# Kernel optimization log

Hardware: AMD Instinct MI355X
Metric: run time of the kernel (lower is better)

## Reference

```python
import jax, jax.numpy as jnp
import numpy as np

B, S, E, H = 4, 2048, 1024, 16
D = E // H  # head dim = 64


def setup_inputs() -> dict:
    key = jax.random.key(0)
    ks = jax.random.split(key, 9)
    s_in = 1.0 / np.sqrt(E)
    return {
        "x": jax.random.normal(ks[0], (B, S, E), dtype=jnp.float32),
        # stacked per-head projection weights, acting as x @ W + b
        "Wq": jax.random.normal(ks[1], (H, E, D), dtype=jnp.float32) * s_in,
        "bq": jax.random.normal(ks[2], (H, D), dtype=jnp.float32) * 0.01,
        "Wk": jax.random.normal(ks[3], (H, E, D), dtype=jnp.float32) * s_in,
        "bk": jax.random.normal(ks[4], (H, D), dtype=jnp.float32) * 0.01,
        "Wv": jax.random.normal(ks[5], (H, E, D), dtype=jnp.float32) * s_in,
        "bv": jax.random.normal(ks[6], (H, D), dtype=jnp.float32) * 0.01,
        "Wo": jax.random.normal(ks[7], (E, E), dtype=jnp.float32) * s_in,
        "bo": jax.random.normal(ks[8], (E,), dtype=jnp.float32) * 0.01,
    }


def reference(x, Wq, bq, Wk, bk, Wv, bv, Wo, bo):
    # Batched per-head projections (equivalent to the per-head nn.Linear loop)
    q = jnp.einsum("bse,hed->bhsd", x, Wq) + bq[None, :, None, :]
    k = jnp.einsum("bse,hed->bhsd", x, Wk) + bk[None, :, None, :]
    v = jnp.einsum("bse,hed->bhsd", x, Wv) + bv[None, :, None, :]
    scale = 1.0 / jnp.sqrt(jnp.asarray(D, dtype=x.dtype))
    scores = jnp.einsum("bhsd,bhtd->bhst", q, k) * scale  # [B,H,S,S]
    attn = jax.nn.softmax(scores, axis=-1)
    ctx = jnp.einsum("bhst,bhtd->bhsd", attn, v)  # [B,H,S,D]
    # torch.cat over heads along last dim -> [B,S,H*D]=[B,S,E]
    ctx = jnp.transpose(ctx, (0, 2, 1, 3)).reshape(x.shape[0], x.shape[1], E)
    return ctx @ Wo + bo
```

## Files before the change

### kernel.cpp

```cpp
#include <hip/hip_runtime.h>
#include <math.h>

#define B_ 4
#define S_ 2048
#define E_ 1024
#define H_ 16
#define D_ 64
#define BH_ (B_ * H_)

#define SCALE_LOG2E 0.18033688011112042f

typedef short short8 __attribute__((ext_vector_type(8)));
typedef float f32x4 __attribute__((ext_vector_type(4)));

static __device__ __forceinline__ unsigned short f2bf(float f) {
    unsigned int u = __float_as_uint(f);
    unsigned int r = (u + 0x7fffu + ((u >> 16) & 1u)) >> 16;
    return (unsigned short)r;
}

static __device__ __forceinline__ unsigned int pack_bf16_trunc(float hi, float lo) {
    return __builtin_amdgcn_perm(__float_as_uint(hi), __float_as_uint(lo), 0x07060302u);
}

static __device__ __forceinline__ void gl_lds16(const unsigned short* g, unsigned short* l) {
    __builtin_amdgcn_global_load_lds(
        (const __attribute__((address_space(1))) unsigned int*)g,
        (__attribute__((address_space(3))) unsigned int*)l, 16, 0, 0);
}


__global__ __launch_bounds__(256) void xcvt_kernel(
    const float* __restrict__ x, unsigned short* __restrict__ Xb)
{
    size_t i = ((size_t)blockIdx.x * 256 + threadIdx.x) * 8;
    float4 a = *(const float4*)&x[i];
    float4 b = *(const float4*)&x[i + 4];
    ushort4 u0, u1;
    u0.x = f2bf(a.x); u0.y = f2bf(a.y); u0.z = f2bf(a.z); u0.w = f2bf(a.w);
    u1.x = f2bf(b.x); u1.y = f2bf(b.y); u1.z = f2bf(b.z); u1.w = f2bf(b.w);
    *(ushort4*)&Xb[i]     = u0;
    *(ushort4*)&Xb[i + 4] = u1;
}

__global__ __launch_bounds__(256) void wtrans_kernel(
    const float* __restrict__ src, unsigned short* __restrict__ dst,
    int R, int C, int srcZ, int dstZ, float scale)
{
    __shared__ float t[32][33];
    const int tx = threadIdx.x & 31, ty = threadIdx.x >> 5;
    const int r0 = blockIdx.x * 32, c0 = blockIdx.y * 32, z = blockIdx.z;
    const float* s = src + (size_t)z * srcZ;
    unsigned short* d = dst + (size_t)z * dstZ;
#pragma unroll
    for (int i = 0; i < 4; ++i)
        t[ty + i * 8][tx] = s[(size_t)(r0 + ty + i * 8) * C + c0 + tx];
    __syncthreads();
#pragma unroll
    for (int i = 0; i < 4; ++i)
        d[(size_t)(c0 + ty + i * 8) * R + r0 + tx] = f2bf(t[tx][ty + i * 8] * scale);
}

__global__ __launch_bounds__(256) void qkv_gemm_kernel(
    const unsigned short* __restrict__ Xb, const unsigned short* __restrict__ Wt,
    const float* __restrict__ bq, const float* __restrict__ bk,
    const float* __restrict__ bv,
    unsigned short* __restrict__ Qh, unsigned short* __restrict__ Kh,
    unsigned short* __restrict__ Vth)
{
    __shared__ unsigned short As[2][128 * 64];
    __shared__ unsigned short Bs[2][128 * 64];
    const int tid = threadIdx.x;
    const int lane = tid & 63, wid = tid >> 6;
    const int quad = lane >> 4, lc = lane & 15;
    const int wm = wid >> 1, wn = wid & 1;
    const int m0 = blockIdx.y * 128, n0 = blockIdx.x * 128;
    const int l8 = lane >> 3;
    const int sch = ((lane & 7) ^ l8) * 8;

    f32x4 acc[4][4];
#pragma unroll
    for (int mt = 0; mt < 4; ++mt)
#pragma unroll
        for (int nt = 0; nt < 4; ++nt)
            acc[mt][nt] = (f32x4){0.f, 0.f, 0.f, 0.f};

#pragma unroll
    for (int i = 0; i < 4; ++i) {
        int rw = wid * 32 + i * 8;
        gl_lds16(&Xb[(size_t)(m0 + rw + l8) * E_ + sch], &As[0][rw * 64]);
        gl_lds16(&Wt[(size_t)(n0 + rw + l8) * E_ + sch], &Bs[0][rw * 64]);
    }
    __syncthreads();

    for (int k0 = 0; k0 < E_; k0 += 64) {
        const int cur = (k0 >> 6) & 1;
        if (k0 + 64 < E_) {
#pragma unroll
            for (int i = 0; i < 4; ++i) {
                int rw = wid * 32 + i * 8;
                gl_lds16(&Xb[(size_t)(m0 + rw + l8) * E_ + k0 + 64 + sch], &As[cur ^ 1][rw * 64]);
                gl_lds16(&Wt[(size_t)(n0 + rw + l8) * E_ + k0 + 64 + sch], &Bs[cur ^ 1][rw * 64]);
            }
        }
#pragma unroll
        for (int kc = 0; kc < 2; ++kc) {
            short8 a[4], bfr[4];
#pragma unroll
            for (int mt = 0; mt < 4; ++mt)
                a[mt] = *(const short8*)&As[cur][(wm * 64 + mt * 16 + lc) * 64 +
                                                (((kc * 4 + quad) ^ (lc & 7)) << 3)];
#pragma unroll
            for (int nt = 0; nt < 4; ++nt)
                bfr[nt] = *(const short8*)&Bs[cur][(wn * 64 + nt * 16 + lc) * 64 +
                                                  (((kc * 4 + quad) ^ (lc & 7)) << 3)];
#pragma unroll
            for (int mt = 0; mt < 4; ++mt)
#pragma unroll
                for (int nt = 0; nt < 4; ++nt)
                    acc[mt][nt] = __builtin_amdgcn_mfma_f32_16x16x32_bf16(
                        a[mt], bfr[nt], acc[mt][nt], 0, 0, 0);
        }
        __syncthreads();
    }

    const int nb = n0 + wn * 64;
    const int mtx = nb >> 10;
    const int h = (nb >> 6) & 15;
    const int sg0 = m0 + wm * 64;
    const int bb_ = sg0 >> 11;
    if (mtx < 2) {
        const float bsc = (mtx == 0) ? SCALE_LOG2E : 1.0f;
        const float* bias = (mtx == 0 ? bq : bk) + h * D_;
        unsigned short* Out = (mtx == 0) ? Qh : Kh;
#pragma unroll
        for (int nt = 0; nt < 4; ++nt) {
            int d = nt * 16 + lc;
            float bb = bias[d] * bsc;
#pragma unroll
            for (int mt = 0; mt < 4; ++mt)
#pragma unroll
                for (int r = 0; r < 4; ++r) {
                    int ss = (sg0 + mt * 16 + quad * 4 + r) & (S_ - 1);
                    Out[((size_t)(bb_ * H_ + h) * S_ + ss) * D_ + d] =
                        f2bf(acc[mt][nt][r] + bb);
                }
        }
    } else {
        const float* bias = bv + h * D_;
#pragma unroll
        for (int nt = 0; nt < 4; ++nt) {
            int d = nt * 16 + lc;
            float bb = bias[d];
#pragma unroll
            for (int mt = 0; mt < 4; ++mt) {
                int ss0 = (sg0 + mt * 16 + quad * 4) & (S_ - 1);
                ushort4 u;
                u.x = f2bf(acc[mt][nt][0] + bb);
                u.y = f2bf(acc[mt][nt][1] + bb);
                u.z = f2bf(acc[mt][nt][2] + bb);
                u.w = f2bf(acc[mt][nt][3] + bb);
                *(ushort4*)&Vth[(((size_t)bb_ * H_ + h) * D_ + d) * S_ + ss0] = u;
            }
        }
    }
}

__global__ __launch_bounds__(256) void attn_kernel(
    const unsigned short* __restrict__ Qh, const unsigned short* __restrict__ Kh,
    const unsigned short* __restrict__ Vth, unsigned short* __restrict__ Ch)
{
    __shared__ unsigned short ps[256 * 64];
    __shared__ unsigned short ks[2][64 * 64];
    __shared__ unsigned short vt[2][64 * 64];
    const int tid = threadIdx.x;
    const int lane = tid & 63, wid = tid >> 6;
    const int quad = lane >> 4, lc = lane & 15;
    const int bh = blockIdx.x, b = bh >> 4, h = bh & 15;
    const int q0 = blockIdx.y * 256;
    const size_t base  = (size_t)bh * S_ * D_;
    const size_t vbase = (size_t)bh * D_ * S_;
    const int l8 = lane >> 3;
    const int sch = ((lane & 7) ^ l8) * 8;

#pragma unroll
    for (int i = 0; i < 8; ++i) {
        int rw = wid * 64 + i * 8;
        gl_lds16(&Qh[base + (size_t)(q0 + rw + l8) * D_ + sch], &ps[rw * 64]);
    }
#pragma unroll
    for (int i = 0; i < 2; ++i) {
        int rw = wid * 16 + i * 8;
        gl_lds16(&Kh[base + (size_t)(rw + l8) * D_ + sch], &ks[0][rw * 64]);
        gl_lds16(&Vth[vbase + (size_t)(rw + l8) * S_ + sch], &vt[0][rw * 64]);
    }
    __syncthreads();
    short8 qf[4][2];
#pragma unroll
    for (int mt = 0; mt < 4; ++mt)
#pragma unroll
        for (int kc = 0; kc < 2; ++kc)
            qf[mt][kc] = *(const short8*)&ps[(wid * 64 + mt * 16 + lc) * 64 +
                                             (((kc * 4 + quad) ^ (lc & 7)) << 3)];

    short8 ones;
#pragma unroll
    for (int i = 0; i < 8; ++i) ones[i] = (short)0x3F80;

    f32x4 ctx[4][4], lacc[4];
#pragma unroll
    for (int mt = 0; mt < 4; ++mt) {
        lacc[mt] = (f32x4){0.f, 0.f, 0.f, 0.f};
#pragma unroll
        for (int nt = 0; nt < 4; ++nt)
            ctx[mt][nt] = (f32x4){0.f, 0.f, 0.f, 0.f};
    }

    for (int kt = 0; kt < S_; kt += 64) {
        const int cur = (kt >> 6) & 1;
        if (kt + 64 < S_) {
#pragma unroll
            for (int i = 0; i < 2; ++i) {
                int rw = wid * 16 + i * 8;
                gl_lds16(&Kh[base + (size_t)(kt + 64 + rw + l8) * D_ + sch],
                         &ks[cur ^ 1][rw * 64]);
                gl_lds16(&Vth[vbase + (size_t)(rw + l8) * S_ + kt + 64 + sch],
                         &vt[cur ^ 1][rw * 64]);
            }
        }

        f32x4 st[4][4];
#pragma unroll
        for (int mtK = 0; mtK < 4; ++mtK)
#pragma unroll
            for (int ntQ = 0; ntQ < 4; ++ntQ)
                st[mtK][ntQ] = (f32x4){0.f, 0.f, 0.f, 0.f};
#pragma unroll
        for (int kc = 0; kc < 2; ++kc) {
            short8 kf[4];
#pragma unroll
            for (int mtK = 0; mtK < 4; ++mtK)
                kf[mtK] = *(const short8*)&ks[cur][(mtK * 16 + lc) * 64 +
                                                  (((kc * 4 + quad) ^ (lc & 7)) << 3)];
#pragma unroll
            for (int mtK = 0; mtK < 4; ++mtK)
#pragma unroll
                for (int ntQ = 0; ntQ < 4; ++ntQ)
                    st[mtK][ntQ] = __builtin_amdgcn_mfma_f32_16x16x32_bf16(
                        kf[mtK], qf[ntQ][kc], st[mtK][ntQ], 0, 0, 0);
        }

#pragma unroll
        for (int ntQ = 0; ntQ < 4; ++ntQ) {
            const int prow = (wid * 64 + ntQ * 16 + lc) * 64 + ((quad & 1) << 2);
#pragma unroll
            for (int mtK = 0; mtK < 4; ++mtK) {
                float p0 = __builtin_amdgcn_exp2f(st[mtK][ntQ][0]);
                float p1 = __builtin_amdgcn_exp2f(st[mtK][ntQ][1]);
                float p2 = __builtin_amdgcn_exp2f(st[mtK][ntQ][2]);
                float p3 = __builtin_amdgcn_exp2f(st[mtK][ntQ][3]);
                uint2 pk;
                pk.x = pack_bf16_trunc(p1, p0);
                pk.y = pack_bf16_trunc(p3, p2);
                *(uint2*)&ps[prow + (((mtK * 2 + (quad >> 1)) ^ (lc & 7)) << 3)] = pk;
            }
        }

#pragma unroll
        for (int kc = 0; kc < 2; ++kc) {
            short8 pf[4], vf[4];
#pragma unroll
            for (int mt = 0; mt < 4; ++mt)
                pf[mt] = *(const short8*)&ps[(wid * 64 + mt * 16 + lc) * 64 +
                                             (((kc * 4 + quad) ^ (lc & 7)) << 3)];
#pragma unroll
            for (int nt = 0; nt < 4; ++nt)
                vf[nt] = *(const short8*)&vt[cur][(nt * 16 + lc) * 64 +
                                                 (((kc * 4 + quad) ^ (lc & 7)) << 3)];
#pragma unroll
            for (int mt = 0; mt < 4; ++mt) {
#pragma unroll
                for (int nt = 0; nt < 4; ++nt)
                    ctx[mt][nt] = __builtin_amdgcn_mfma_f32_16x16x32_bf16(
                        pf[mt], vf[nt], ctx[mt][nt], 0, 0, 0);
                lacc[mt] = __builtin_amdgcn_mfma_f32_16x16x32_bf16(
                    pf[mt], ones, lacc[mt], 0, 0, 0);
            }
        }
        __syncthreads();
    }

#pragma unroll
    for (int mt = 0; mt < 4; ++mt) {
#pragma unroll
        for (int r = 0; r < 4; ++r) {
            float inv = 1.f / lacc[mt][r];
            int row = q0 + wid * 64 + mt * 16 + quad * 4 + r;
#pragma unroll
            for (int nt = 0; nt < 4; ++nt)
                Ch[((size_t)b * S_ + row) * E_ + h * D_ + nt * 16 + lc] =
                    f2bf(ctx[mt][nt][r] * inv);
        }
    }
}

__global__ __launch_bounds__(256) void out_proj_kernel(
    const unsigned short* __restrict__ Ch, const unsigned short* __restrict__ Wot,
    const float* __restrict__ bo, float* __restrict__ out)
{
    __shared__ unsigned short As[2][128 * 64];
    __shared__ unsigned short Bs[2][128 * 64];
    const int tid = threadIdx.x;
    const int lane = tid & 63, wid = tid >> 6;
    const int quad = lane >> 4, lc = lane & 15;
    const int wm = wid >> 1, wn = wid & 1;
    const int m0 = blockIdx.y * 128, n0 = blockIdx.x * 128;
    const int l8 = lane >> 3;
    const int sch = ((lane & 7) ^ l8) * 8;

    f32x4 acc[4][4];
#pragma unroll
    for (int mt = 0; mt < 4; ++mt)
#pragma unroll
        for (int nt = 0; nt < 4; ++nt)
            acc[mt][nt] = (f32x4){0.f, 0.f, 0.f, 0.f};

#pragma unroll
    for (int i = 0; i < 4; ++i) {
        int rw = wid * 32 + i * 8;
        gl_lds16(&Ch[(size_t)(m0 + rw + l8) * E_ + sch], &As[0][rw * 64]);
        gl_lds16(&Wot[(size_t)(n0 + rw + l8) * E_ + sch], &Bs[0][rw * 64]);
    }
    __syncthreads();

    for (int k0 = 0; k0 < E_; k0 += 64) {
        const int cur = (k0 >> 6) & 1;
        if (k0 + 64 < E_) {
#pragma unroll
            for (int i = 0; i < 4; ++i) {
                int rw = wid * 32 + i * 8;
                gl_lds16(&Ch[(size_t)(m0 + rw + l8) * E_ + k0 + 64 + sch], &As[cur ^ 1][rw * 64]);
                gl_lds16(&Wot[(size_t)(n0 + rw + l8) * E_ + k0 + 64 + sch], &Bs[cur ^ 1][rw * 64]);
            }
        }
#pragma unroll
        for (int kc = 0; kc < 2; ++kc) {
            short8 a[4], bfr[4];
#pragma unroll
            for (int mt = 0; mt < 4; ++mt)
                a[mt] = *(const short8*)&As[cur][(wm * 64 + mt * 16 + lc) * 64 +
                                                (((kc * 4 + quad) ^ (lc & 7)) << 3)];
#pragma unroll
            for (int nt = 0; nt < 4; ++nt)
                bfr[nt] = *(const short8*)&Bs[cur][(wn * 64 + nt * 16 + lc) * 64 +
                                                  (((kc * 4 + quad) ^ (lc & 7)) << 3)];
#pragma unroll
            for (int mt = 0; mt < 4; ++mt)
#pragma unroll
                for (int nt = 0; nt < 4; ++nt)
                    acc[mt][nt] = __builtin_amdgcn_mfma_f32_16x16x32_bf16(
                        a[mt], bfr[nt], acc[mt][nt], 0, 0, 0);
        }
        __syncthreads();
    }

#pragma unroll
    for (int mt = 0; mt < 4; ++mt)
#pragma unroll
        for (int nt = 0; nt < 4; ++nt) {
            int n = n0 + wn * 64 + nt * 16 + lc;
            float bb = bo[n];
#pragma unroll
            for (int r = 0; r < 4; ++r) {
                int row = m0 + wm * 64 + mt * 16 + quad * 4 + r;
                out[(size_t)row * E_ + n] = acc[mt][nt][r] + bb;
            }
        }
}

extern "C" void kernel_launch(void* const* d_in, const int* in_sizes, int n_in,
                              void* d_out, int out_size, void* d_ws, size_t ws_size,
                              hipStream_t stream)
{
    const float* x  = (const float*)d_in[0];
    const float* Wq = (const float*)d_in[1];
    const float* bq = (const float*)d_in[2];
    const float* Wk = (const float*)d_in[3];
    const float* bk = (const float*)d_in[4];
    const float* Wv = (const float*)d_in[5];
    const float* bv = (const float*)d_in[6];
    const float* Wo = (const float*)d_in[7];
    const float* bo = (const float*)d_in[8];
    (void)in_sizes; (void)n_in; (void)out_size; (void)ws_size;

    const size_t N = (size_t)BH_ * S_ * D_;
    unsigned short* Wt  = (unsigned short*)d_ws;
    unsigned short* Wot = Wt + (size_t)3072 * 1024;
    unsigned short* Xb  = Wot + (size_t)1024 * 1024;
    unsigned short* Qh  = Xb + N;
    unsigned short* Kh  = Qh + N;
    unsigned short* Vth = Kh + N;
    unsigned short* Ch  = Vth + N;

    xcvt_kernel<<<dim3(4096), 256, 0, stream>>>(x, Xb);
    wtrans_kernel<<<dim3(32, 2, 16), 256, 0, stream>>>(Wq, Wt,                   E_, D_, E_ * D_, D_ * E_, SCALE_LOG2E);
    wtrans_kernel<<<dim3(32, 2, 16), 256, 0, stream>>>(Wk, Wt + 1024 * 1024,     E_, D_, E_ * D_, D_ * E_, 1.0f);
    wtrans_kernel<<<dim3(32, 2, 16), 256, 0, stream>>>(Wv, Wt + 2 * 1024 * 1024, E_, D_, E_ * D_, D_ * E_, 1.0f);
    wtrans_kernel<<<dim3(32, 32, 1), 256, 0, stream>>>(Wo, Wot, E_, E_, 0, 0, 1.0f);

    qkv_gemm_kernel<<<dim3(24, 64), 256, 0, stream>>>(Xb, Wt, bq, bk, bv, Qh, Kh, Vth);
    attn_kernel<<<dim3(64, 8), 256, 0, stream>>>(Qh, Kh, Vth, Ch);
    out_proj_kernel<<<dim3(8, 64), 256, 0, stream>>>(Ch, Wot, bo, (float*)d_out);
}
```

Measured before the change: 277.4 us.

## Load attention K/V/Q fragments directly from global memory and merge QKV weight transposes

The attention kernel drops its double-buffered LDS staging of K and V tiles and loads Q, K and V MFMA fragments straight from global memory into registers. This removes the per-iteration block barrier and about 32 KB of LDS, and the kernel now requests two blocks per CU. The cost is that each wave reads the same K/V data separately through the cache with no explicit prefetch, so global latency is exposed within each iteration. Separately, the three Q/K/V weight-transpose launches are merged into one launch.

```diff
diff --git a/kernel.cpp b/kernel.cpp
--- a/kernel.cpp
+++ b/kernel.cpp
@@ -43,22 +43,39 @@
     *(ushort4*)&Xb[i + 4] = u1;
 }
 
-__global__ __launch_bounds__(256) void wtrans_kernel(
-    const float* __restrict__ src, unsigned short* __restrict__ dst,
-    int R, int C, int srcZ, int dstZ, float scale)
+__global__ __launch_bounds__(256) void wtrans_qkv_kernel(
+    const float* __restrict__ Wq, const float* __restrict__ Wk,
+    const float* __restrict__ Wv, unsigned short* __restrict__ Wt)
 {
     __shared__ float t[32][33];
     const int tx = threadIdx.x & 31, ty = threadIdx.x >> 5;
-    const int r0 = blockIdx.x * 32, c0 = blockIdx.y * 32, z = blockIdx.z;
-    const float* s = src + (size_t)z * srcZ;
-    unsigned short* d = dst + (size_t)z * dstZ;
+    const int r0 = blockIdx.x * 32, c0 = blockIdx.y * 32;
+    const int z = blockIdx.z, mtx = z >> 4, h = z & 15;
+    const float* s = (mtx == 0 ? Wq : (mtx == 1 ? Wk : Wv)) + (size_t)h * E_ * D_;
+    const float scale = (mtx == 0) ? SCALE_LOG2E : 1.0f;
+    unsigned short* d = Wt + (size_t)mtx * E_ * E_ + (size_t)h * D_ * E_;
 #pragma unroll
     for (int i = 0; i < 4; ++i)
-        t[ty + i * 8][tx] = s[(size_t)(r0 + ty + i * 8) * C + c0 + tx];
+        t[ty + i * 8][tx] = s[(size_t)(r0 + ty + i * 8) * D_ + c0 + tx];
     __syncthreads();
 #pragma unroll
     for (int i = 0; i < 4; ++i)
-        d[(size_t)(c0 + ty + i * 8) * R + r0 + tx] = f2bf(t[tx][ty + i * 8] * scale);
+        d[(size_t)(c0 + ty + i * 8) * E_ + r0 + tx] = f2bf(t[tx][ty + i * 8] * scale);
+}
+
+__global__ __launch_bounds__(256) void wtrans_kernel(
+    const float* __restrict__ src, unsigned short* __restrict__ dst, int R, int C)
+{
+    __shared__ float t[32][33];
+    const int tx = threadIdx.x & 31, ty = threadIdx.x >> 5;
+    const int r0 = blockIdx.x * 32, c0 = blockIdx.y * 32;
+#pragma unroll
+    for (int i = 0; i < 4; ++i)
+        t[ty + i * 8][tx] = src[(size_t)(r0 + ty + i * 8) * C + c0 + tx];
+    __syncthreads();
+#pragma unroll
+    for (int i = 0; i < 4; ++i)
+        dst[(size_t)(c0 + ty + i * 8) * R + r0 + tx] = f2bf(t[tx][ty + i * 8]);
 }
 
 __global__ __launch_bounds__(256) void qkv_gemm_kernel(
@@ -166,13 +183,11 @@
     }
 }
 
-__global__ __launch_bounds__(256) void attn_kernel(
+__global__ __launch_bounds__(256, 2) void attn_kernel(
     const unsigned short* __restrict__ Qh, const unsigned short* __restrict__ Kh,
     const unsigned short* __restrict__ Vth, unsigned short* __restrict__ Ch)
 {
     __shared__ unsigned short ps[256 * 64];
-    __shared__ unsigned short ks[2][64 * 64];
-    __shared__ unsigned short vt[2][64 * 64];
     const int tid = threadIdx.x;
     const int lane = tid & 63, wid = tid >> 6;
     const int quad = lane >> 4, lc = lane & 15;
@@ -180,28 +195,14 @@
     const int q0 = blockIdx.y * 256;
     const size_t base  = (size_t)bh * S_ * D_;
     const size_t vbase = (size_t)bh * D_ * S_;
-    const int l8 = lane >> 3;
-    const int sch = ((lane & 7) ^ l8) * 8;
-
-#pragma unroll
-    for (int i = 0; i < 8; ++i) {
-        int rw = wid * 64 + i * 8;
-        gl_lds16(&Qh[base + (size_t)(q0 + rw + l8) * D_ + sch], &ps[rw * 64]);
-    }
-#pragma unroll
-    for (int i = 0; i < 2; ++i) {
-        int rw = wid * 16 + i * 8;
-        gl_lds16(&Kh[base + (size_t)(rw + l8) * D_ + sch], &ks[0][rw * 64]);
-        gl_lds16(&Vth[vbase + (size_t)(rw + l8) * S_ + sch], &vt[0][rw * 64]);
-    }
-    __syncthreads();
+
     short8 qf[4][2];
 #pragma unroll
     for (int mt = 0; mt < 4; ++mt)
 #pragma unroll
         for (int kc = 0; kc < 2; ++kc)
-            qf[mt][kc] = *(const short8*)&ps[(wid * 64 + mt * 16 + lc) * 64 +
-                                             (((kc * 4 + quad) ^ (lc & 7)) << 3)];
+            qf[mt][kc] = *(const short8*)&Qh[base +
+                (size_t)(q0 + wid * 64 + mt * 16 + lc) * D_ + kc * 32 + quad * 8];
 
     short8 ones;
 #pragma unroll
@@ -217,17 +218,13 @@
     }
 
     for (int kt = 0; kt < S_; kt += 64) {
-        const int cur = (kt >> 6) & 1;
-        if (kt + 64 < S_) {
-#pragma unroll
-            for (int i = 0; i < 2; ++i) {
-                int rw = wid * 16 + i * 8;
-                gl_lds16(&Kh[base + (size_t)(kt + 64 + rw + l8) * D_ + sch],
-                         &ks[cur ^ 1][rw * 64]);
-                gl_lds16(&Vth[vbase + (size_t)(rw + l8) * S_ + kt + 64 + sch],
-                         &vt[cur ^ 1][rw * 64]);
-            }
-        }
+        short8 kf[4][2];
+#pragma unroll
+        for (int mtK = 0; mtK < 4; ++mtK)
+#pragma unroll
+            for (int kc = 0; kc < 2; ++kc)
+                kf[mtK][kc] = *(const short8*)&Kh[base +
+                    (size_t)(kt + mtK * 16 + lc) * D_ + kc * 32 + quad * 8];
 
         f32x4 st[4][4];
 #pragma unroll
@@ -236,19 +233,21 @@
             for (int ntQ = 0; ntQ < 4; ++ntQ)
                 st[mtK][ntQ] = (f32x4){0.f, 0.f, 0.f, 0.f};
 #pragma unroll
-        for (int kc = 0; kc < 2; ++kc) {
-            short8 kf[4];
-#pragma unroll
-            for (int mtK = 0; mtK < 4; ++mtK)
-                kf[mtK] = *(const short8*)&ks[cur][(mtK * 16 + lc) * 64 +
-                                                  (((kc * 4 + quad) ^ (lc & 7)) << 3)];
+        for (int kc = 0; kc < 2; ++kc)
 #pragma unroll
             for (int mtK = 0; mtK < 4; ++mtK)
 #pragma unroll
                 for (int ntQ = 0; ntQ < 4; ++ntQ)
                     st[mtK][ntQ] = __builtin_amdgcn_mfma_f32_16x16x32_bf16(
-                        kf[mtK], qf[ntQ][kc], st[mtK][ntQ], 0, 0, 0);
-        }
+                        kf[mtK][kc], qf[ntQ][kc], st[mtK][ntQ], 0, 0, 0);
+
+        short8 vf[4][2];
+#pragma unroll
+        for (int nt = 0; nt < 4; ++nt)
+#pragma unroll
+            for (int kc = 0; kc < 2; ++kc)
+                vf[nt][kc] = *(const short8*)&Vth[vbase +
+                    (size_t)(nt * 16 + lc) * S_ + kt + kc * 32 + quad * 8];
 
 #pragma unroll
         for (int ntQ = 0; ntQ < 4; ++ntQ) {
@@ -268,26 +267,21 @@
 
 #pragma unroll
         for (int kc = 0; kc < 2; ++kc) {
-            short8 pf[4], vf[4];
+            short8 pf[4];
 #pragma unroll
             for (int mt = 0; mt < 4; ++mt)
                 pf[mt] = *(const short8*)&ps[(wid * 64 + mt * 16 + lc) * 64 +
                                              (((kc * 4 + quad) ^ (lc & 7)) << 3)];
 #pragma unroll
-            for (int nt = 0; nt < 4; ++nt)
-                vf[nt] = *(const short8*)&vt[cur][(nt * 16 + lc) * 64 +
-                                                 (((kc * 4 + quad) ^ (lc & 7)) << 3)];
-#pragma unroll
             for (int mt = 0; mt < 4; ++mt) {
 #pragma unroll
                 for (int nt = 0; nt < 4; ++nt)
                     ctx[mt][nt] = __builtin_amdgcn_mfma_f32_16x16x32_bf16(
-                        pf[mt], vf[nt], ctx[mt][nt], 0, 0, 0);
+                        pf[mt], vf[nt][kc], ctx[mt][nt], 0, 0, 0);
                 lacc[mt] = __builtin_amdgcn_mfma_f32_16x16x32_bf16(
                     pf[mt], ones, lacc[mt], 0, 0, 0);
             }
         }
-        __syncthreads();
     }
 
 #pragma unroll
@@ -403,10 +397,8 @@
     unsigned short* Ch  = Vth + N;
 
     xcvt_kernel<<<dim3(4096), 256, 0, stream>>>(x, Xb);
-    wtrans_kernel<<<dim3(32, 2, 16), 256, 0, stream>>>(Wq, Wt,                   E_, D_, E_ * D_, D_ * E_, SCALE_LOG2E);
-    wtrans_kernel<<<dim3(32, 2, 16), 256, 0, stream>>>(Wk, Wt + 1024 * 1024,     E_, D_, E_ * D_, D_ * E_, 1.0f);
-    wtrans_kernel<<<dim3(32, 2, 16), 256, 0, stream>>>(Wv, Wt + 2 * 1024 * 1024, E_, D_, E_ * D_, D_ * E_, 1.0f);
-    wtrans_kernel<<<dim3(32, 32, 1), 256, 0, stream>>>(Wo, Wot, E_, E_, 0, 0, 1.0f);
+    wtrans_qkv_kernel<<<dim3(32, 2, 48), 256, 0, stream>>>(Wq, Wk, Wv, Wt);
+    wtrans_kernel<<<dim3(32, 32, 1), 256, 0, stream>>>(Wo, Wot, E_, E_);
 
     qkv_gemm_kernel<<<dim3(24, 64), 256, 0, stream>>>(Xb, Wt, bq, bk, bv, Qh, Kh, Vth);
     attn_kernel<<<dim3(64, 8), 256, 0, stream>>>(Qh, Kh, Vth, Ch);
```

Measured after the change: 319.5 us. 1.15x slower.
